# Kernel tuning notes

Measured on AMD Instinct MI355X. Metric: run time of the kernel, lower is better.

Reference implementation:

```python
import jax, jax.numpy as jnp
import numpy as np

B, S, N_IN, N_OUT = 4, 192, 256, 1

def setup_inputs() -> dict:
    key = jax.random.key(0)
    ks = jax.random.split(key, 7)
    scale = 1.0 / np.sqrt(N_IN)
    return {
        "h_head": jax.random.normal(ks[0], (B, S, N_IN), jnp.float32),
        "h_dep": jax.random.normal(ks[1], (B, S, N_IN), jnp.float32),
        "h_sib": jax.random.normal(ks[2], (B, S, N_IN), jnp.float32),
        "W_tri": jax.random.normal(ks[3], (N_OUT, N_IN, N_IN, N_IN), jnp.float32) * (scale / N_IN),
        "U_hd": jax.random.normal(ks[4], (N_OUT, N_IN, N_IN), jnp.float32) * scale,
        "V_hs": jax.random.normal(ks[5], (N_OUT, N_IN, N_IN), jnp.float32) * scale,
        "Z_ds": jax.random.normal(ks[6], (N_OUT, N_IN, N_IN), jnp.float32) * scale,
        "bias": jnp.zeros((N_OUT,), jnp.float32),
    }

def reference(h_head, h_dep, h_sib, W_tri, U_hd, V_hs, Z_ds, bias):
    # biaffine terms: [b, x, y, o]
    s_hd = jnp.einsum('bhi,oij,bdj->bhdo', h_head, U_hd, h_dep)
    s_hs = jnp.einsum('bhi,oij,bsj->bhso', h_head, V_hs, h_sib)
    s_ds = jnp.einsum('bdi,oij,bsj->bdso', h_dep, Z_ds, h_sib)
    # trilinear term: note j,k of W_tri appear nowhere else, so they are
    # reduced first (w_red[o,i] = sum_{j,k} W_tri[o,i,j,k]) — same math as
    # torch.einsum('bhi,bdi,bsi,oijk->bhdso', ...).
    w_red = jnp.sum(W_tri, axis=(2, 3))  # [o, i]
    s_tri = jnp.einsum('bhi,bdi,bsi,oi->bhdso', h_head, h_dep, h_sib, w_red)
    scores = (s_tri
              + s_hd[:, :, :, None, :]   # unsqueeze sib axis
              + s_hs[:, :, None, :, :]   # unsqueeze dep axis
              + s_ds[:, None, :, :, :]   # unsqueeze head axis
              + bias)
    return scores[..., 0]  # n_out == 1 -> squeeze last dim
```

## Files before the change

### kernel.cpp

```cpp
#include <hip/hip_runtime.h>
#include <hip/hip_fp16.h>
#include <stdint.h>

#define NB 4
#define SS 192
#define NI 256

typedef __attribute__((ext_vector_type(8))) _Float16 f16x8;
typedef __attribute__((ext_vector_type(2))) __fp16 fp16v2;
typedef __attribute__((ext_vector_type(16))) float f32x16;

__device__ __forceinline__ uint16_t f2h(float f) {
  union { _Float16 h; uint16_t u; } t; t.h = (_Float16)f; return t.u;
}

__device__ __forceinline__ uint32_t cvt2(float lo, float hi) {
  union { fp16v2 h; uint32_t u; } t;
  t.h = __builtin_amdgcn_cvt_pkrtz(lo, hi);
  return t.u;
}

__device__ __forceinline__ uint4 pack8h(const float4 a, const float4 b) {
  uint4 r;
  r.x = cvt2(a.x, a.y);
  r.y = cvt2(a.z, a.w);
  r.z = cvt2(b.x, b.y);
  r.w = cvt2(b.z, b.w);
  return r;
}

__device__ __forceinline__ uint32_t hmul2(uint32_t x, uint32_t y) {
  union { uint32_t u; __half2 h; } a, b, c;
  a.u = x; b.u = y;
  c.h = __hmul2(a.h, b.h);
  return c.u;
}


__global__ __launch_bounds__(256) void kA(
    const float* __restrict__ W,
    const float* __restrict__ h_head, const float* __restrict__ h_dep, const float* __restrict__ h_sib,
    const float* __restrict__ U, const float* __restrict__ V, const float* __restrict__ Z,
    float* __restrict__ partial,
    uint16_t* __restrict__ HH, uint16_t* __restrict__ HD, uint16_t* __restrict__ HS,
    uint16_t* __restrict__ dU16, uint16_t* __restrict__ T216, uint16_t* __restrict__ TZ16) {
  const int bi = blockIdx.x, tid = threadIdx.x;

  if (bi >= 120) {
    __shared__ float red[4];
    const int c = bi - 120;
    const float4* pw = (const float4*)(W + (size_t)c * 8192);
    float4 a = {0.f, 0.f, 0.f, 0.f};
    #pragma unroll
    for (int it = 0; it < 8; ++it) {
      const float4 v = pw[it * 256 + tid];
      a.x += v.x; a.y += v.y; a.z += v.z; a.w += v.w;
    }
    float s = (a.x + a.y) + (a.z + a.w);
    for (int off = 32; off > 0; off >>= 1) s += __shfl_down(s, off, 64);
    if ((tid & 63) == 0) red[tid >> 6] = s;
    __syncthreads();
    if (tid == 0) partial[c] = red[0] + red[1] + red[2] + red[3];
    return;
  }
  if (bi >= 24) {
    const int rl = tid >> 5, c8 = tid & 31;
    const int g = (bi - 24) * 8 + rl;
    const int dst = g * 32 + (c8 ^ (g & 15));
    const int srci = g * 64 + c8 * 2;
    { const float4 x = ((const float4*)h_head)[srci], y = ((const float4*)h_head)[srci + 1];
      ((uint4*)HH)[dst] = pack8h(x, y); }
    { const float4 x = ((const float4*)h_dep)[srci], y = ((const float4*)h_dep)[srci + 1];
      ((uint4*)HD)[dst] = pack8h(x, y); }
    { const float4 x = ((const float4*)h_sib)[srci], y = ((const float4*)h_sib)[srci + 1];
      ((uint4*)HS)[dst] = pack8h(x, y); }
    return;
  }

  {
    __shared__ __align__(16) uint16_t Ah[192 * 128];
    __shared__ __align__(16) uint16_t Bh[128 * 128];
    const int which = bi >> 3, rem = bi & 7;
    const int b = rem >> 1, nt = rem & 1;
    const float* As = (which == 0) ? h_dep : h_sib;
    const float* Bs = (which == 0) ? U : (which == 1) ? V : Z;
    uint16_t* Os = (which == 0) ? dU16 : (which == 1) ? T216 : TZ16;
    const int lane = tid & 63, w = tid >> 6;
    const int l31 = lane & 31, l5 = lane >> 5;
    const int N0 = nt * 128;
    f32x16 acc[6] = {};

    #pragma unroll
    for (int kh = 0; kh < 2; ++kh) {
      const int kbase = kh * 128;
      if (kh) __syncthreads();
      #pragma unroll
      for (int i = 0; i < 12; ++i) {
        const int slot = i * 256 + tid;
        const int row = slot >> 4, ck = slot & 15;
        const float* sp = As + (size_t)(b * SS + row) * NI + kbase + ck * 8;
        const float4 x = *(const float4*)sp, y = *(const float4*)(sp + 4);
        *(uint4*)((char*)Ah + row * 256 + ((ck ^ (row & 15)) << 4)) = pack8h(x, y);
      }
      #pragma unroll
      for (int i = 0; i < 8; ++i) {
        const int slot = i * 256 + tid;
        const int row = slot >> 4, ck = slot & 15;
        const float* sp = Bs + (size_t)(N0 + row) * NI + kbase + ck * 8;
        const float4 x = *(const float4*)sp, y = *(const float4*)(sp + 4);
        *(uint4*)((char*)Bh + row * 256 + ((ck ^ (row & 15)) << 4)) = pack8h(x, y);
      }
      __syncthreads();
      const int brow = w * 32 + l31;
      const int bbyte = brow * 256;
      const int bmask = brow & 15;
      #pragma unroll
      for (int ks = 0; ks < 8; ++ks) {
        const int sl = ks * 2 + l5;
        f16x8 bf = *reinterpret_cast<const f16x8*>((const char*)Bh + bbyte + ((sl ^ bmask) << 4));
        #pragma unroll
        for (int mt = 0; mt < 6; ++mt) {
          const int ar = mt * 32 + l31;
          f16x8 af = *reinterpret_cast<const f16x8*>((const char*)Ah + ar * 256 + ((sl ^ (ar & 15)) << 4));
          acc[mt] = __builtin_amdgcn_mfma_f32_32x32x16_f16(af, bf, acc[mt], 0, 0, 0);
        }
      }
    }
    const int n = N0 + w * 32 + l31;
    const int nck = n >> 3, npos = n & 7;
    #pragma unroll
    for (int mt = 0; mt < 6; ++mt) {
      #pragma unroll
      for (int r = 0; r < 16; ++r) {
        const int m = mt * 32 + (r & 3) + 8 * (r >> 2) + 4 * l5;
        Os[(size_t)(b * SS + m) * NI + ((nck ^ (m & 15)) << 3) + npos] = f2h(acc[mt][r]);
      }
    }
  }
}

__global__ __launch_bounds__(384, 1) void k_s2(
    const uint16_t* __restrict__ HH, const uint16_t* __restrict__ HD,
    const uint16_t* __restrict__ dU16, const uint16_t* __restrict__ T216, const uint16_t* __restrict__ TZ16,
    float* __restrict__ s_hd, float* __restrict__ s_hs, float* __restrict__ s_ds) {
  __shared__ __align__(16) uint16_t Ah[192 * 128];
  __shared__ __align__(16) uint16_t Bh[192 * 128];
  const int which = blockIdx.x, b = blockIdx.y;
  const uint16_t* As = (which == 2) ? HD : HH;
  const uint16_t* Bs = (which == 0) ? dU16 : (which == 1) ? T216 : TZ16;
  float* Os = (which == 0) ? s_hd : (which == 1) ? s_hs : s_ds;
  const int tid = threadIdx.x, lane = tid & 63, w = tid >> 6;
  const int l31 = lane & 31, l5 = lane >> 5;
  f32x16 acc[6] = {};

  #pragma unroll
  for (int kh = 0; kh < 2; ++kh) {
    const int kbase = kh * 128;
    if (kh) __syncthreads();
    #pragma unroll
    for (int i = 0; i < 8; ++i) {
      const int slot = i * 384 + tid;
      const int row = slot >> 4, ck = slot & 15;
      const uint16_t* src = As + (size_t)(b * SS + row) * NI + kbase + ck * 8;
      __builtin_amdgcn_global_load_lds((const __attribute__((address_space(1))) void*)src,
          (__attribute__((address_space(3))) void*)(Ah + (size_t)slot * 8), 16, 0, 0);
    }
    #pragma unroll
    for (int i = 0; i < 8; ++i) {
      const int slot = i * 384 + tid;
      const int row = slot >> 4, ck = slot & 15;
      const uint16_t* src = Bs + (size_t)(b * SS + row) * NI + kbase + ck * 8;
      __builtin_amdgcn_global_load_lds((const __attribute__((address_space(1))) void*)src,
          (__attribute__((address_space(3))) void*)(Bh + (size_t)slot * 8), 16, 0, 0);
    }
    __syncthreads();
    const int brow = w * 32 + l31;
    const int bbyte = brow * 256;
    const int bmask = brow & 15;
    #pragma unroll
    for (int ks = 0; ks < 8; ++ks) {
      const int sl = ks * 2 + l5;
      f16x8 bf = *reinterpret_cast<const f16x8*>((const char*)Bh + bbyte + ((sl ^ bmask) << 4));
      #pragma unroll
      for (int mt = 0; mt < 6; ++mt) {
        const int ar = mt * 32 + l31;
        f16x8 af = *reinterpret_cast<const f16x8*>((const char*)Ah + ar * 256 + ((sl ^ (ar & 15)) << 4));
        acc[mt] = __builtin_amdgcn_mfma_f32_32x32x16_f16(af, bf, acc[mt], 0, 0, 0);
      }
    }
  }
  const int n = w * 32 + l31;
  #pragma unroll
  for (int mt = 0; mt < 6; ++mt) {
    #pragma unroll
    for (int r = 0; r < 16; ++r) {
      const int m = mt * 32 + (r & 3) + 8 * (r >> 2) + 4 * l5;
      Os[(size_t)(b * SS + m) * SS + n] = acc[mt][r];
    }
  }
}

__global__ __launch_bounds__(576) void k3_big(
    const uint16_t* __restrict__ HH, const uint16_t* __restrict__ HS,
    const float* __restrict__ h_dep, const float* __restrict__ partial,
    const float* __restrict__ s_hd, const float* __restrict__ s_hs,
    const float* __restrict__ s_ds,
    const float* __restrict__ bias, float* __restrict__ out) {
  __shared__ __align__(16) uint16_t Btile[96 * 128];
  __shared__ __align__(16) uint16_t Atile[96 * 128];
  __shared__ uint16_t cvec[NI];
  __shared__ float chd_s[96];
  const int d = blockIdx.x, hb = blockIdx.y >> 1, sb = blockIdx.y & 1, b = blockIdx.z;
  const int tid = threadIdx.x;
  const int lane = tid & 63, w = tid >> 6;
  const int wh = w / 3, ws = w % 3;
  const int l31 = lane & 31, l5 = lane >> 5;

  if (tid < NI) {
    float wr = 0.f;
    #pragma unroll
    for (int q = 0; q < 8; ++q) wr += partial[8 * tid + q];
    cvec[tid] = f2h(wr * h_dep[(b * SS + d) * NI + tid]);
  } else if (tid < NI + 96) {
    const int t = tid - NI;
    chd_s[t] = s_hd[(size_t)(b * SS + hb * 96 + t) * SS + d];
  }
  __syncthreads();

  f32x16 acc = {};

  #pragma unroll
  for (int half = 0; half < 2; ++half) {
    const int kbase = half * 128;
    if (half) __syncthreads();
    #pragma unroll
    for (int i = 0; i < 3; ++i) {
      const int slot = i * 576 + tid;
      if (slot < 1536) {
        const int row = slot >> 4;
        const uint16_t* src = HS + ((size_t)(b * SS + sb * 96 + row) << 8) + kbase + (slot & 15) * 8;
        __builtin_amdgcn_global_load_lds(
            (const __attribute__((address_space(1))) void*)src,
            (__attribute__((address_space(3))) void*)(Btile + (size_t)slot * 8),
            16, 0, 0);
      }
    }
    #pragma unroll
    for (int i = 0; i < 3; ++i) {
      const int slot = i * 576 + tid;
      if (slot < 1536) {
        const int row = slot >> 4;
        const int kc = slot & 15;
        const int lcl = kc ^ (row & 15);
        const uint4 cv4 = *(const uint4*)(cvec + kbase + lcl * 8);
        const uint4 hh4 = *(const uint4*)(HH + ((size_t)(b * SS + hb * 96 + row) << 8) + kbase + kc * 8);
        uint4 a4;
        a4.x = hmul2(hh4.x, cv4.x);
        a4.y = hmul2(hh4.y, cv4.y);
        a4.z = hmul2(hh4.z, cv4.z);
        a4.w = hmul2(hh4.w, cv4.w);
        *(uint4*)((char*)Atile + (size_t)slot * 16) = a4;
      }
    }
    __syncthreads();
    const int arow = wh * 32 + l31;
    const int abyte = arow * 256;
    const int amask = arow & 15;
    const int brow = ws * 32 + l31;
    const int bbyte = brow * 256;
    const int bmask = brow & 15;
    #pragma unroll
    for (int ks = 0; ks < 8; ++ks) {
      const int sl = ks * 2 + l5;
      f16x8 af = *reinterpret_cast<const f16x8*>((const char*)Atile + abyte + ((sl ^ amask) << 4));
      f16x8 bf = *reinterpret_cast<const f16x8*>((const char*)Btile + bbyte + ((sl ^ bmask) << 4));
      acc = __builtin_amdgcn_mfma_f32_32x32x16_f16(af, bf, acc, 0, 0, 0);
    }
  }

  const float bias0 = bias[0];
  const int s = sb * 96 + ws * 32 + l31;
  const float dsv = s_ds[(b * SS + d) * SS + s];
  #pragma unroll
  for (int r = 0; r < 16; ++r) {
    const int hl = wh * 32 + (r & 3) + 8 * (r >> 2) + 4 * l5;
    const float v = acc[r] + chd_s[hl] + bias0
                  + s_hs[(size_t)(b * SS + hb * 96 + hl) * SS + s] + dsv;
    out[((size_t)(b * SS + hb * 96 + hl) * SS + d) * SS + s] = v;
  }
}

extern "C" void kernel_launch(void* const* d_in, const int* in_sizes, int n_in,
                              void* d_out, int out_size, void* d_ws, size_t ws_size,
                              hipStream_t stream) {
  const float* h_head = (const float*)d_in[0];
  const float* h_dep  = (const float*)d_in[1];
  const float* h_sib  = (const float*)d_in[2];
  const float* W_tri  = (const float*)d_in[3];
  const float* U_hd   = (const float*)d_in[4];
  const float* V_hs   = (const float*)d_in[5];
  const float* Z_ds   = (const float*)d_in[6];
  const float* bias   = (const float*)d_in[7];
  float* out = (float*)d_out;

  float* ws = (float*)d_ws;
  float* partial = ws;          ws += 2048;
  float* s_hd    = ws;          ws += NB * SS * SS;
  float* s_hs    = ws;          ws += NB * SS * SS;
  float* s_ds    = ws;          ws += NB * SS * SS;
  uint16_t* HH   = (uint16_t*)ws;
  uint16_t* HD   = HH + NB * SS * NI;
  uint16_t* HS   = HD + NB * SS * NI;
  uint16_t* dU16 = HS + NB * SS * NI;
  uint16_t* T216 = dU16 + NB * SS * NI;
  uint16_t* TZ16 = T216 + NB * SS * NI;

  kA<<<2168, 256, 0, stream>>>(W_tri, h_head, h_dep, h_sib, U_hd, V_hs, Z_ds,
                               partial, HH, HD, HS, dU16, T216, TZ16);
  k_s2<<<dim3(3, NB), 384, 0, stream>>>(HH, HD, dU16, T216, TZ16, s_hd, s_hs, s_ds);
  k3_big<<<dim3(SS, 4, NB), 576, 0, stream>>>(HH, HS, h_dep, partial,
                                              s_hd, s_hs, s_ds, bias, out);
}
```

Measured before the change: 65.51 us.

## Process four dep indices per block, reusing full HH/HS tiles in LDS

Each k3_big block now loads the full 96x256 head and sib half-precision tiles into LDS once and loops over four dep indices, so the grid shrinks by a factor of four. The c-vector scaling of HH moves from the tile-staging phase into the MFMA inner loop, applied per fragment with packed multiplies. The change is meant to cut redundant global loads and block-launch overhead. In exchange it uses more LDS per block, which may lower occupancy, and the dd loop serializes four MFMA chains with their output stores inside each block.

```diff
diff --git a/kernel.cpp b/kernel.cpp
--- a/kernel.cpp
+++ b/kernel.cpp
@@ -206,87 +206,83 @@
     const float* __restrict__ s_hd, const float* __restrict__ s_hs,
     const float* __restrict__ s_ds,
     const float* __restrict__ bias, float* __restrict__ out) {
-  __shared__ __align__(16) uint16_t Btile[96 * 128];
-  __shared__ __align__(16) uint16_t Atile[96 * 128];
-  __shared__ uint16_t cvec[NI];
-  __shared__ float chd_s[96];
-  const int d = blockIdx.x, hb = blockIdx.y >> 1, sb = blockIdx.y & 1, b = blockIdx.z;
+  __shared__ __align__(16) uint16_t HHt[96 * 256];
+  __shared__ __align__(16) uint16_t HSt[96 * 256];
+  __shared__ __align__(16) uint16_t cvec4[4 * 256];
+  __shared__ float chd4[4][96];
+  __shared__ float sds4[4][96];
+  const int d0 = blockIdx.x * 4, hb = blockIdx.y >> 1, sb = blockIdx.y & 1, b = blockIdx.z;
   const int tid = threadIdx.x;
   const int lane = tid & 63, w = tid >> 6;
   const int wh = w / 3, ws = w % 3;
   const int l31 = lane & 31, l5 = lane >> 5;
 
+  #pragma unroll
+  for (int i = 0; i < 11; ++i) {
+    const int slot = i * 576 + tid;
+    if (slot < 3072) {
+      const int row = slot >> 5, c = slot & 31;
+      const uint16_t* src = HH + ((size_t)(b * SS + hb * 96 + row) << 8) + c * 8;
+      __builtin_amdgcn_global_load_lds((const __attribute__((address_space(1))) void*)src,
+          (__attribute__((address_space(3))) void*)(HHt + (size_t)slot * 8), 16, 0, 0);
+    } else if (slot < 6144) {
+      const int s2 = slot - 3072;
+      const int row = s2 >> 5, c = s2 & 31;
+      const uint16_t* src = HS + ((size_t)(b * SS + sb * 96 + row) << 8) + c * 8;
+      __builtin_amdgcn_global_load_lds((const __attribute__((address_space(1))) void*)src,
+          (__attribute__((address_space(3))) void*)(HSt + (size_t)s2 * 8), 16, 0, 0);
+    }
+  }
   if (tid < NI) {
     float wr = 0.f;
     #pragma unroll
     for (int q = 0; q < 8; ++q) wr += partial[8 * tid + q];
-    cvec[tid] = f2h(wr * h_dep[(b * SS + d) * NI + tid]);
-  } else if (tid < NI + 96) {
-    const int t = tid - NI;
-    chd_s[t] = s_hd[(size_t)(b * SS + hb * 96 + t) * SS + d];
+    #pragma unroll
+    for (int dd = 0; dd < 4; ++dd)
+      cvec4[dd * NI + tid] = f2h(wr * h_dep[(size_t)(b * SS + d0 + dd) * NI + tid]);
+  }
+  if (tid < 384) {
+    const int dd = tid / 96, t = tid % 96;
+    chd4[dd][t] = s_hd[(size_t)(b * SS + hb * 96 + t) * SS + (d0 + dd)];
+    sds4[dd][t] = s_ds[(size_t)(b * SS + d0 + dd) * SS + sb * 96 + t];
   }
   __syncthreads();
 
-  f32x16 acc = {};
-
-  #pragma unroll
-  for (int half = 0; half < 2; ++half) {
-    const int kbase = half * 128;
-    if (half) __syncthreads();
-    #pragma unroll
-    for (int i = 0; i < 3; ++i) {
-      const int slot = i * 576 + tid;
-      if (slot < 1536) {
-        const int row = slot >> 4;
-        const uint16_t* src = HS + ((size_t)(b * SS + sb * 96 + row) << 8) + kbase + (slot & 15) * 8;
-        __builtin_amdgcn_global_load_lds(
-            (const __attribute__((address_space(1))) void*)src,
-            (__attribute__((address_space(3))) void*)(Btile + (size_t)slot * 8),
-            16, 0, 0);
-      }
-    }
-    #pragma unroll
-    for (int i = 0; i < 3; ++i) {
-      const int slot = i * 576 + tid;
-      if (slot < 1536) {
-        const int row = slot >> 4;
-        const int kc = slot & 15;
-        const int lcl = kc ^ (row & 15);
-        const uint4 cv4 = *(const uint4*)(cvec + kbase + lcl * 8);
-        const uint4 hh4 = *(const uint4*)(HH + ((size_t)(b * SS + hb * 96 + row) << 8) + kbase + kc * 8);
-        uint4 a4;
-        a4.x = hmul2(hh4.x, cv4.x);
-        a4.y = hmul2(hh4.y, cv4.y);
-        a4.z = hmul2(hh4.z, cv4.z);
-        a4.w = hmul2(hh4.w, cv4.w);
-        *(uint4*)((char*)Atile + (size_t)slot * 16) = a4;
-      }
-    }
-    __syncthreads();
-    const int arow = wh * 32 + l31;
-    const int abyte = arow * 256;
-    const int amask = arow & 15;
-    const int brow = ws * 32 + l31;
-    const int bbyte = brow * 256;
-    const int bmask = brow & 15;
-    #pragma unroll
-    for (int ks = 0; ks < 8; ++ks) {
-      const int sl = ks * 2 + l5;
-      f16x8 af = *reinterpret_cast<const f16x8*>((const char*)Atile + abyte + ((sl ^ amask) << 4));
-      f16x8 bf = *reinterpret_cast<const f16x8*>((const char*)Btile + bbyte + ((sl ^ bmask) << 4));
-      acc = __builtin_amdgcn_mfma_f32_32x32x16_f16(af, bf, acc, 0, 0, 0);
-    }
-  }
-
   const float bias0 = bias[0];
-  const int s = sb * 96 + ws * 32 + l31;
-  const float dsv = s_ds[(b * SS + d) * SS + s];
-  #pragma unroll
-  for (int r = 0; r < 16; ++r) {
-    const int hl = wh * 32 + (r & 3) + 8 * (r >> 2) + 4 * l5;
-    const float v = acc[r] + chd_s[hl] + bias0
-                  + s_hs[(size_t)(b * SS + hb * 96 + hl) * SS + s] + dsv;
-    out[((size_t)(b * SS + hb * 96 + hl) * SS + d) * SS + s] = v;
+  const int arow = wh * 32 + l31, amask = arow & 15;
+  const int brow = ws * 32 + l31, bmask = brow & 15;
+  const int abase = arow * 512;
+  const int bbase = brow * 512;
+  const int sloc = ws * 32 + l31;
+  const int s = sb * 96 + sloc;
+
+  for (int dd = 0; dd < 4; ++dd) {
+    f32x16 acc = {};
+    #pragma unroll
+    for (int kh = 0; kh < 2; ++kh) {
+      #pragma unroll
+      for (int ks = 0; ks < 8; ++ks) {
+        const int sl = ks * 2 + l5;
+        union { f16x8 v; uint4 u; } A, C, R;
+        A.v = *reinterpret_cast<const f16x8*>((const char*)HHt + abase + kh * 256 + ((sl ^ amask) << 4));
+        C.v = *reinterpret_cast<const f16x8*>((const char*)cvec4 + dd * 512 + kh * 256 + (sl << 4));
+        R.u.x = hmul2(A.u.x, C.u.x);
+        R.u.y = hmul2(A.u.y, C.u.y);
+        R.u.z = hmul2(A.u.z, C.u.z);
+        R.u.w = hmul2(A.u.w, C.u.w);
+        const f16x8 bf = *reinterpret_cast<const f16x8*>((const char*)HSt + bbase + kh * 256 + ((sl ^ bmask) << 4));
+        acc = __builtin_amdgcn_mfma_f32_32x32x16_f16(R.v, bf, acc, 0, 0, 0);
+      }
+    }
+    const int d = d0 + dd;
+    const float dsv = sds4[dd][sloc];
+    #pragma unroll
+    for (int r = 0; r < 16; ++r) {
+      const int hl = wh * 32 + (r & 3) + 8 * (r >> 2) + 4 * l5;
+      const float v = acc[r] + chd4[dd][hl] + bias0
+                    + s_hs[(size_t)(b * SS + hb * 96 + hl) * SS + s] + dsv;
+      out[((size_t)(b * SS + hb * 96 + hl) * SS + d) * SS + s] = v;
+    }
   }
 }
 
@@ -318,6 +314,6 @@
   kA<<<2168, 256, 0, stream>>>(W_tri, h_head, h_dep, h_sib, U_hd, V_hs, Z_ds,
                                partial, HH, HD, HS, dU16, T216, TZ16);
   k_s2<<<dim3(3, NB), 384, 0, stream>>>(HH, HD, dU16, T216, TZ16, s_hd, s_hs, s_ds);
-  k3_big<<<dim3(SS, 4, NB), 576, 0, stream>>>(HH, HS, h_dep, partial,
+  k3_big<<<dim3(48, 4, NB), 576, 0, stream>>>(HH, HS, h_dep, partial,
                                               s_hd, s_hs, s_ds, bias, out);
 }
```

Result: slower. 75.06 us (+14.6%).
